# Kernel optimization log

Hardware: AMD Instinct MI355X
Metric: run time of the kernel (lower is better)

## Reference

```python
import jax, jax.numpy as jnp
import numpy as np

N, E, B = 25000, 400000, 64          # nodes, edges, graphs
F, ED, H, C = 32, 8, 4, 32           # feature/edge dims, heads, per-head dim
HC = H * C
L = 4                                # init conv + 3 stacked convs (same shapes)
LIN = 128


def setup_inputs() -> dict:
    key = jax.random.key(0)
    ks = jax.random.split(key, 24)
    s = 0.05
    inp = {
        "x": jax.random.normal(ks[0], (N, F), jnp.float32),
        "edge_attr": jax.random.normal(ks[1], (E, ED), jnp.float32),
        "edge_index": jax.random.randint(ks[2], (2, E), 0, N),
        "batch_index": jnp.sort(jax.random.randint(ks[3], (N,), 0, B)),
        # stacked TransformerConv params (leading dim = layer)
        "Wq": jax.random.normal(ks[4], (L, F, HC), jnp.float32) * s,
        "bq": jnp.zeros((L, HC), jnp.float32),
        "Wk": jax.random.normal(ks[5], (L, F, HC), jnp.float32) * s,
        "bk": jnp.zeros((L, HC), jnp.float32),
        "Wv": jax.random.normal(ks[6], (L, F, HC), jnp.float32) * s,
        "bv": jnp.zeros((L, HC), jnp.float32),
        "We": jax.random.normal(ks[7], (L, ED, HC), jnp.float32) * s,
        "be": jnp.zeros((L, HC), jnp.float32),
        "Wskip": jax.random.normal(ks[8], (L, F, HC), jnp.float32) * s,
        "bskip": jnp.zeros((L, HC), jnp.float32),
        "Wbeta": jax.random.normal(ks[9], (L, 3 * HC, 1), jnp.float32) * s,
        # per-layer Linear(H*C -> emb) + BatchNorm
        "Wlin": jax.random.normal(ks[10], (L, HC, F), jnp.float32) * s,
        "blin": jnp.zeros((L, F), jnp.float32),
        "bn_gamma": jnp.ones((L, F), jnp.float32),
        "bn_beta": jnp.zeros((L, F), jnp.float32),
        # readout MLP
        "W1": jax.random.normal(ks[11], (2 * F, LIN), jnp.float32) * s,
        "b1": jnp.zeros((LIN,), jnp.float32),
        "W2": jax.random.normal(ks[12], (LIN, LIN // 2), jnp.float32) * s,
        "b2": jnp.zeros((LIN // 2,), jnp.float32),
        "W3": jax.random.normal(ks[13], (LIN // 2, 1), jnp.float32) * s,
        "b3": jnp.zeros((1,), jnp.float32),
    }
    return inp


def _transformer_conv(x, edge_attr, src, dst, Wq, bq, Wk, bk, Wv, bv, We, be,
                      Wskip, bskip, Wbeta):
    """PyG TransformerConv(heads=H, concat=True, beta=True, edge_dim=ED), eval mode."""
    n = x.shape[0]
    q = (x @ Wq + bq).reshape(n, H, C)
    k = (x @ Wk + bk).reshape(n, H, C)
    v = (x @ Wv + bv).reshape(n, H, C)
    e = (edge_attr @ We + be).reshape(-1, H, C)          # [E,H,C]
    kj = k[src] + e                                       # key_j + edge
    alpha = jnp.einsum('ehc,ehc->eh', q[dst], kj) / np.sqrt(C).astype(np.float32)
    # segment softmax over incoming edges per destination node
    amax = jax.ops.segment_max(alpha, dst, num_segments=n)
    a = jnp.exp(alpha - amax[dst])
    denom = jax.ops.segment_sum(a, dst, num_segments=n)
    a = a / denom[dst]                                    # [E,H]
    msg = (v[src] + e) * a[:, :, None]
    out = jax.ops.segment_sum(msg, dst, num_segments=n).reshape(n, HC)
    x_skip = x @ Wskip + bskip
    beta = jax.nn.sigmoid(
        jnp.concatenate([out, x_skip, out - x_skip], axis=-1) @ Wbeta)  # [N,1]
    return beta * x_skip + (1.0 - beta) * out


def _bn(h, gamma, beta):
    m = h.mean(axis=0)
    v = h.var(axis=0)
    return (h - m) * jax.lax.rsqrt(v + 1e-5) * gamma + beta


def reference(x, edge_attr, edge_index, batch_index,
              Wq, bq, Wk, bk, Wv, bv, We, be, Wskip, bskip, Wbeta,
              Wlin, blin, bn_gamma, bn_beta, W1, b1, W2, b2, W3, b3):
    src, dst = edge_index[0], edge_index[1]
    counts = jax.ops.segment_sum(jnp.ones((N,), jnp.float32), batch_index,
                                 num_segments=B)[:, None]
    h = x
    rep = jnp.zeros((B, 2 * F), jnp.float32)
    for i in range(L):
        h = _transformer_conv(h, edge_attr, src, dst,
                              Wq[i], bq[i], Wk[i], bk[i], Wv[i], bv[i],
                              We[i], be[i], Wskip[i], bskip[i], Wbeta[i])
        h = jax.nn.elu(h @ Wlin[i] + blin[i])
        h = _bn(h, bn_gamma[i], bn_beta[i])
        if i > 0:  # original pools only inside the n_layers loop
            gmx = jax.ops.segment_max(h, batch_index, num_segments=B)
            gmean = jax.ops.segment_sum(h, batch_index, num_segments=B) / counts
            rep = rep + jnp.concatenate([gmx, gmean], axis=1)
    z = jax.nn.elu(rep @ W1 + b1)
    z = jax.nn.elu(z @ W2 + b2)
    return z @ W3 + b3  # [B,1]
```

## Files before the change

### kernel.cpp

```cpp
#include <hip/hip_runtime.h>
#include <hip/hip_bf16.h>
#include <hip/hip_fp16.h>
#include <math.h>

#define NN 25000
#define EE 400000
#define BB 64
#define FF 32
#define EDD 8
#define HH 4
#define CC 32
#define HCC 128
#define LL 4
#define LINN 128

#define RSQRT_C 0.17677669529663687f
#define NREP 16
#define LSTATS_WORDS (NREP * 64)


__global__ void deg_kernel(const int* __restrict__ dst, int* __restrict__ deg) {
    int i = blockIdx.x * blockDim.x + threadIdx.x;
    if (i < EE) atomicAdd(&deg[dst[i]], 1);
}

__global__ void gstart_kernel(const int* __restrict__ bidx, int* __restrict__ gstart) {
    int b = threadIdx.x;
    if (b <= BB) {
        int lo = 0, hi = NN;
        while (lo < hi) { int mid = (lo + hi) >> 1; if (bidx[mid] < b) lo = mid + 1; else hi = mid; }
        gstart[b] = lo;
    }
}

__global__ void scan1_kernel(const int* __restrict__ deg, int* __restrict__ rowp, int* __restrict__ blks) {
    __shared__ int s[256];
    int i = blockIdx.x * 256 + threadIdx.x;
    int v = (i < NN) ? deg[i] : 0;
    s[threadIdx.x] = v;
    __syncthreads();
    for (int off = 1; off < 256; off <<= 1) {
        int t = (threadIdx.x >= off) ? s[threadIdx.x - off] : 0;
        __syncthreads();
        s[threadIdx.x] += t;
        __syncthreads();
    }
    if (i < NN) rowp[i + 1] = s[threadIdx.x];
    if (threadIdx.x == 255) blks[blockIdx.x] = s[255];
    if (i == 0) rowp[0] = 0;
}

__global__ void scan2_kernel(int* __restrict__ blks, int nb) {
    __shared__ int s[128];
    int t = threadIdx.x;
    int v = (t < nb) ? blks[t] : 0;
    s[t] = v;
    __syncthreads();
    for (int off = 1; off < 128; off <<= 1) {
        int u = (t >= off) ? s[t - off] : 0;
        __syncthreads();
        s[t] += u;
        __syncthreads();
    }
    if (t < nb) blks[t] = s[t] - v;
}

__global__ void scan3_kernel(int* __restrict__ rowp, const int* __restrict__ blks) {
    int i = blockIdx.x * 256 + threadIdx.x;
    if (i < NN) rowp[i + 1] += blks[blockIdx.x];
}

__global__ void fill_kernel(const int* __restrict__ dst, const int* __restrict__ rowp,
                            int* __restrict__ cnt2, int* __restrict__ eid) {
    int i = blockIdx.x * blockDim.x + threadIdx.x;
    if (i < EE) {
        int d = dst[i];
        int pos = rowp[d] + atomicAdd(&cnt2[d], 1);
        eid[pos] = i;
    }
}

__global__ void sortseg_kernel(const int* __restrict__ rowp, int* __restrict__ eid) {
    int n = blockIdx.x * 256 + threadIdx.x;
    if (n >= NN) return;
    int b = rowp[n], e = rowp[n + 1];
    int d = e - b;
    if (d <= 1) return;
    if (d <= 64) {
        int buf[64];
        for (int i = 0; i < d; ++i) buf[i] = eid[b + i];
        for (int i = 1; i < d; ++i) {
            int key = buf[i];
            int j = i - 1;
            while (j >= 0 && buf[j] > key) { buf[j + 1] = buf[j]; --j; }
            buf[j + 1] = key;
        }
        for (int i = 0; i < d; ++i) eid[b + i] = buf[i];
    } else {
        for (int i = b + 1; i < e; ++i) {
            int key = eid[i];
            int j = i - 1;
            while (j >= b && eid[j] > key) { eid[j + 1] = eid[j]; --j; }
            eid[j + 1] = key;
        }
    }
}

__global__ void csr_gather_kernel(const int* __restrict__ csre, const int* __restrict__ srcA,
                                  const float* __restrict__ eattr,
                                  int* __restrict__ csrsrc, float4* __restrict__ ecsr) {
    int j = blockIdx.x * blockDim.x + threadIdx.x;
    if (j < EE) {
        int e = csre[j];
        csrsrc[j] = srcA[e];
        const float4* s = (const float4*)(eattr + (size_t)e * 8);
        ecsr[(size_t)j * 2] = s[0];
        ecsr[(size_t)j * 2 + 1] = s[1];
    }
}

__global__ __launch_bounds__(256) void qkvs_kernel(
    const float* __restrict__ hin,
    const float* __restrict__ Wq, const float* __restrict__ bq,
    const float* __restrict__ Wk, const float* __restrict__ bk,
    const float* __restrict__ Wv, const float* __restrict__ bv,
    const float* __restrict__ Ws, const float* __restrict__ bs,
    float2* __restrict__ qo,
    __half2* __restrict__ kvo,
    float2* __restrict__ so, float* __restrict__ lstats)
{
    if (blockIdx.x == 0) {
        for (int i = threadIdx.x; i < LSTATS_WORDS; i += 256) lstats[i] = 0.0f;
    }
    __shared__ float xs[32][32];
    int lane = threadIdx.x & 63;
    int sel = threadIdx.x >> 6;
    const float* W = (sel == 0) ? Wq : (sel == 1) ? Wk : (sel == 2) ? Wv : Ws;
    const float* bias = (sel == 0) ? bq : (sel == 1) ? bk : (sel == 2) ? bv : bs;
    float w0[32], w1[32];
#pragma unroll
    for (int f = 0; f < 32; ++f) {
        float2 t = *(const float2*)&W[f * 128 + 2 * lane];
        w0[f] = t.x; w1[f] = t.y;
    }
    float2 bvv = *(const float2*)&bias[2 * lane];

    int c = lane >> 1;
    int pr = lane & 1;
    int f2idx = c * 2 + pr;
    int h2k   = c * 4 + pr;
    int h2v   = c * 4 + 2 + pr;

    for (int chunk = blockIdx.x * 32; chunk < NN; chunk += gridDim.x * 32) {
        __syncthreads();
        for (int i = threadIdx.x; i < 1024; i += 256) {
            int nn = chunk + (i >> 5);
            xs[i >> 5][i & 31] = (nn < NN) ? hin[nn * 32 + (i & 31)] : 0.0f;
        }
        __syncthreads();
        int nmax = NN - chunk; if (nmax > 32) nmax = 32;
        for (int nl = 0; nl < nmax; ++nl) {
            float a0 = bvv.x, a1 = bvv.y;
#pragma unroll
            for (int f = 0; f < 32; ++f) {
                float xv = xs[nl][f];
                a0 += xv * w0[f];
                a1 += xv * w1[f];
            }
            size_t node = (size_t)(chunk + nl);
            if (sel == 0)      qo[node * 64 + f2idx] = make_float2(a0, a1);
            else if (sel == 1) kvo[node * 128 + h2k] = __float22half2_rn(make_float2(a0, a1));
            else if (sel == 2) kvo[node * 128 + h2v] = __float22half2_rn(make_float2(a0, a1));
            else               so[node * 64 + f2idx] = make_float2(a0, a1);
        }
    }
}

__global__ __launch_bounds__(256) void attn_kernel(
    const float4* __restrict__ qb4, const uint4* __restrict__ kvb4,
    const float4* __restrict__ skb4,
    const float4* __restrict__ eb4,
    const int* __restrict__ srcArr,
    const int* __restrict__ rowp,
    const float* __restrict__ WeL, const float* __restrict__ beL,
    const float* __restrict__ WbL,
    const float* __restrict__ WlinL, const float* __restrict__ blinL,
    float* __restrict__ hlin, float* __restrict__ bnpart)
{
    __shared__ __align__(16) float shc[4 * 128];
    __shared__ float sbn[64];

    int tid = threadIdx.x;
    if (tid < 64) sbn[tid] = 0.0f;
    __syncthreads();

    int w = tid >> 6;
    int lane = tid & 63;
    int n = blockIdx.x * 4 + w;

    if (n < NN) {
        int c = lane & 31;
        int h = lane >> 5;

        float4 we[8];
#pragma unroll
        for (int d = 0; d < 8; ++d) we[d] = *(const float4*)&WeL[d * 128 + 4 * c];
        float4 be4 = *(const float4*)&beL[4 * c];
        float4 wbo = *(const float4*)&WbL[4 * c];
        float4 wbs = *(const float4*)&WbL[128 + 4 * c];
        float4 wbd = *(const float4*)&WbL[256 + 4 * c];

        float4 q4 = qb4[(size_t)n * 32 + c];
        q4.x *= RSQRT_C; q4.y *= RSQRT_C; q4.z *= RSQRT_C; q4.w *= RSQRT_C;
        float4 sk4 = skb4[(size_t)n * 32 + c];

        int beg = rowp[n], end = rowp[n + 1];
        int cnt = end - beg;
        int last = end - 1;

        float s = 0.0f, a0 = 0.0f, a1 = 0.0f, a2 = 0.0f, a3 = 0.0f;

        uint4 kvA = make_uint4(0u, 0u, 0u, 0u), kvB = kvA;
        float4 eaA0 = make_float4(0.f, 0.f, 0.f, 0.f), eaA1 = eaA0;
        float4 eaB0 = eaA0, eaB1 = eaA0;
        int snC = 0, snD = 0;

        if (cnt > 0) {
            int j0 = beg + h;     j0 = (j0 < end) ? j0 : last;
            int j1 = beg + 2 + h; j1 = (j1 < end) ? j1 : last;
            int j2 = beg + 4 + h; j2 = (j2 < end) ? j2 : last;
            int j3 = beg + 6 + h; j3 = (j3 < end) ? j3 : last;
            int snA = srcArr[j0];
            int snB = srcArr[j1];
            snC = srcArr[j2];
            snD = srcArr[j3];
            kvA  = kvb4[(size_t)snA * 32 + c];
            kvB  = kvb4[(size_t)snB * 32 + c];
            eaA0 = eb4[(size_t)j0 * 2];
            eaA1 = eb4[(size_t)j0 * 2 + 1];
            eaB0 = eb4[(size_t)j1 * 2];
            eaB1 = eb4[(size_t)j1 * 2 + 1];
        }

        for (int jb = beg; jb < end; jb += 2) {
            int j = jb + h;
            uint4 kvC = kvb4[(size_t)snC * 32 + c];
            int jn = (j + 4 < end) ? j + 4 : last;
            float4 eaC0 = eb4[(size_t)jn * 2];
            float4 eaC1 = eb4[(size_t)jn * 2 + 1];
            int j8 = (j + 8 < end) ? j + 8 : last;
            int snE = srcArr[j8];

            float ex = be4.x, ey = be4.y, ez = be4.z, ew = be4.w;
            ex += eaA0.x * we[0].x + eaA0.y * we[1].x + eaA0.z * we[2].x + eaA0.w * we[3].x
                + eaA1.x * we[4].x + eaA1.y * we[5].x + eaA1.z * we[6].x + eaA1.w * we[7].x;
            ey += eaA0.x * we[0].y + eaA0.y * we[1].y + eaA0.z * we[2].y + eaA0.w * we[3].y
                + eaA1.x * we[4].y + eaA1.y * we[5].y + eaA1.z * we[6].y + eaA1.w * we[7].y;
            ez += eaA0.x * we[0].z + eaA0.y * we[1].z + eaA0.z * we[2].z + eaA0.w * we[3].z
                + eaA1.x * we[4].z + eaA1.y * we[5].z + eaA1.z * we[6].z + eaA1.w * we[7].z;
            ew += eaA0.x * we[0].w + eaA0.y * we[1].w + eaA0.z * we[2].w + eaA0.w * we[3].w
                + eaA1.x * we[4].w + eaA1.y * we[5].w + eaA1.z * we[6].w + eaA1.w * we[7].w;

            float2 k01 = __half22float2(*(const __half2*)&kvA.x);
            float2 k23 = __half22float2(*(const __half2*)&kvA.y);
            float2 v01 = __half22float2(*(const __half2*)&kvA.z);
            float2 v23 = __half22float2(*(const __half2*)&kvA.w);

            float p = q4.x * (k01.x + ex) + q4.y * (k01.y + ey)
                    + q4.z * (k23.x + ez) + q4.w * (k23.y + ew);
            p += __shfl_xor(p, 1);
            p += __shfl_xor(p, 2);
            p += __shfl_xor(p, 4);
            float wg = (j < end) ? __expf(p) : 0.0f;
            s += wg;
            a0 = fmaf(wg, v01.x + ex, a0);
            a1 = fmaf(wg, v01.y + ey, a1);
            a2 = fmaf(wg, v23.x + ez, a2);
            a3 = fmaf(wg, v23.y + ew, a3);

            kvA = kvB; kvB = kvC;
            eaA0 = eaB0; eaA1 = eaB1; eaB0 = eaC0; eaB1 = eaC1;
            snC = snD; snD = snE;
        }

        s  += __shfl_xor(s, 32);
        a0 += __shfl_xor(a0, 32);
        a1 += __shfl_xor(a1, 32);
        a2 += __shfl_xor(a2, 32);
        a3 += __shfl_xor(a3, 32);

        float rs = (cnt > 0) ? (1.0f / s) : 0.0f;
        float o0 = a0 * rs, o1 = a1 * rs, o2 = a2 * rs, o3 = a3 * rs;

        float t = o0 * wbo.x + sk4.x * wbs.x + (o0 - sk4.x) * wbd.x
                + o1 * wbo.y + sk4.y * wbs.y + (o1 - sk4.y) * wbd.y
                + o2 * wbo.z + sk4.z * wbs.z + (o2 - sk4.z) * wbd.z
                + o3 * wbo.w + sk4.w * wbs.w + (o3 - sk4.w) * wbd.w;
#pragma unroll
        for (int off = 1; off <= 16; off <<= 1) t += __shfl_xor(t, off);
        float beta = 1.0f / (1.0f + __expf(-t));
        float4 hc4;
        hc4.x = beta * sk4.x + (1.0f - beta) * o0;
        hc4.y = beta * sk4.y + (1.0f - beta) * o1;
        hc4.z = beta * sk4.z + (1.0f - beta) * o2;
        hc4.w = beta * sk4.w + (1.0f - beta) * o3;
        if (h == 0) ((float4*)shc)[w * 32 + c] = hc4;
        int cc = lane & 31;
        int half = lane >> 5;
        float acc = 0.0f;
#pragma unroll 8
        for (int i = 0; i < 64; ++i) {
            int ch = half * 64 + i;
            acc += shc[w * 128 + ch] * WlinL[ch * 32 + cc];
        }
        acc += __shfl_xor(acc, 32);
        if (lane < 32) {
            float hv = acc + blinL[lane];
            hv = (hv > 0.0f) ? hv : expm1f(hv);
            hlin[n * 32 + lane] = hv;
            atomicAdd(&sbn[lane], hv);
            atomicAdd(&sbn[32 + lane], hv * hv);
        }
    }
    __syncthreads();
    if (tid < 64) atomicAdd(&bnpart[(blockIdx.x & (NREP - 1)) * 64 + tid], sbn[tid]);
}

__global__ __launch_bounds__(256) void bnpool_kernel(
    const float* __restrict__ hlin, const float* __restrict__ bnpart,
    const float* __restrict__ gamma, const float* __restrict__ bnbeta,
    const int* __restrict__ gstart,
    float* __restrict__ hc, float* __restrict__ rep, int doPool)
{
    __shared__ float sscale[32], sshift[32];
    __shared__ float smax[8][32], ssum[8][32];
    int tid = threadIdx.x;
    int ch = tid & 31, row = tid >> 5;
    if (tid < 32) {
        float sm = 0.0f, sq = 0.0f;
#pragma unroll
        for (int r = 0; r < NREP; ++r) { sm += bnpart[r * 64 + tid]; sq += bnpart[r * 64 + 32 + tid]; }
        float mean = sm * (1.0f / NN);
        float var = sq * (1.0f / NN) - mean * mean;
        float scale = gamma[tid] * rsqrtf(var + 1e-5f);
        sscale[tid] = scale;
        sshift[tid] = bnbeta[tid] - mean * scale;
    }
    __syncthreads();
    int g = blockIdx.x;
    int gs = gstart[g], ge = gstart[g + 1];
    float scale = sscale[ch], shift = sshift[ch];
    float mx = -1e30f, sum = 0.0f;
    for (int n = gs + row; n < ge; n += 8) {
        float val = hlin[n * 32 + ch] * scale + shift;
        hc[n * 32 + ch] = val;
        mx = fmaxf(mx, val);
        sum += val;
    }
    if (doPool) {
        smax[row][ch] = mx; ssum[row][ch] = sum;
        __syncthreads();
        if (row == 0) {
#pragma unroll
            for (int r = 1; r < 8; ++r) { mx = fmaxf(mx, smax[r][ch]); sum += ssum[r][ch]; }
            int cntg = ge - gs;
            if (cntg > 0) {
                rep[g * 64 + ch]      += mx;
                rep[g * 64 + 32 + ch] += sum / (float)cntg;
            }
        }
    }
}

__device__ __forceinline__ float eluf(float x) { return x > 0.0f ? x : expm1f(x); }

__global__ __launch_bounds__(128) void readout_kernel(
    const float* __restrict__ rep,
    const float* __restrict__ W1, const float* __restrict__ b1,
    const float* __restrict__ W2, const float* __restrict__ b2,
    const float* __restrict__ W3, const float* __restrict__ b3,
    float* __restrict__ out)
{
    __shared__ float sr[64];
    __shared__ float sz1[128];
    __shared__ float sz2[64];
    int g = blockIdx.x;
    int t = threadIdx.x;
    if (t < 64) sr[t] = rep[g * 64 + t];
    __syncthreads();
    float acc = b1[t];
#pragma unroll 8
    for (int i = 0; i < 64; ++i) acc += sr[i] * W1[i * 128 + t];
    sz1[t] = eluf(acc);
    __syncthreads();
    if (t < 64) {
        float a2 = b2[t];
#pragma unroll 8
        for (int i = 0; i < 128; ++i) a2 += sz1[i] * W2[i * 64 + t];
        sz2[t] = eluf(a2);
    }
    __syncthreads();
    if (t < 64) {
        float p = sz2[t] * W3[t];
#pragma unroll
        for (int off = 1; off <= 32; off <<= 1) p += __shfl_xor(p, off);
        if (t == 0) out[g] = p + b3[0];
    }
}


extern "C" void kernel_launch(void* const* d_in, const int* in_sizes, int n_in,
                              void* d_out, int out_size, void* d_ws, size_t ws_size,
                              hipStream_t stream) {
    const float* x      = (const float*)d_in[0];
    const float* eattr  = (const float*)d_in[1];
    const int*   eidx   = (const int*)d_in[2];
    const int*   bidx   = (const int*)d_in[3];
    const float* Wq     = (const float*)d_in[4];
    const float* bq     = (const float*)d_in[5];
    const float* Wk     = (const float*)d_in[6];
    const float* bk     = (const float*)d_in[7];
    const float* Wv     = (const float*)d_in[8];
    const float* bv     = (const float*)d_in[9];
    const float* We     = (const float*)d_in[10];
    const float* be     = (const float*)d_in[11];
    const float* Wskip  = (const float*)d_in[12];
    const float* bskip  = (const float*)d_in[13];
    const float* Wbeta  = (const float*)d_in[14];
    const float* Wlin   = (const float*)d_in[15];
    const float* blin   = (const float*)d_in[16];
    const float* bng    = (const float*)d_in[17];
    const float* bnb    = (const float*)d_in[18];
    const float* W1     = (const float*)d_in[19];
    const float* b1     = (const float*)d_in[20];
    const float* W2     = (const float*)d_in[21];
    const float* b2     = (const float*)d_in[22];
    const float* W3     = (const float*)d_in[23];
    const float* b3     = (const float*)d_in[24];
    float* out = (float*)d_out;

    char* ws = (char*)d_ws;
    size_t off = 0;
    auto alloc = [&](size_t bytes) -> char* {
        char* p = ws + off;
        off = (off + bytes + 255) & ~(size_t)255;
        return p;
    };
    int*    rowp   = (int*)alloc((NN + 1) * 4);
    int*    degcnt = (int*)alloc(2 * NN * 4);
    int*    deg    = degcnt;
    int*    cnt2   = degcnt + NN;
    int*    csre   = (int*)alloc(EE * 4);
    int*    blks   = (int*)alloc(128 * 4);
    int*    gstart = (int*)alloc((BB + 1) * 4);
    float*  rep    = (float*)alloc(BB * 64 * 4);
    float4* qB     = (float4*)alloc((size_t)NN * 32 * 16);
    uint4*  kvB    = (uint4*)alloc((size_t)NN * 32 * 16);
    float4* skB    = (float4*)alloc((size_t)NN * 32 * 16);
    float*  hlin   = (float*)alloc((size_t)NN * 32 * 4);
    float*  hcur   = (float*)alloc((size_t)NN * 32 * 4);
    float*  bnpart = (float*)alloc(LSTATS_WORDS * 4);
    int*    csrsrc = (int*)alloc(EE * 4);
    float4* ecsr   = (float4*)alloc((size_t)EE * 32);

    const int* srcA = eidx;
    const int* dstA = eidx + EE;

    (void)hipMemsetAsync(degcnt, 0, 2 * NN * 4, stream);
    (void)hipMemsetAsync(rep, 0, BB * 64 * 4, stream);

    deg_kernel<<<(EE + 255) / 256, 256, 0, stream>>>(dstA, deg);
    gstart_kernel<<<1, 128, 0, stream>>>(bidx, gstart);
    scan1_kernel<<<98, 256, 0, stream>>>(deg, rowp, blks);
    scan2_kernel<<<1, 128, 0, stream>>>(blks, 98);
    scan3_kernel<<<98, 256, 0, stream>>>(rowp, blks);
    fill_kernel<<<(EE + 255) / 256, 256, 0, stream>>>(dstA, rowp, cnt2, csre);
    sortseg_kernel<<<98, 256, 0, stream>>>(rowp, csre);
    csr_gather_kernel<<<(EE + 255) / 256, 256, 0, stream>>>(csre, srcA, eattr, csrsrc, ecsr);

    const float* hin = x;
    for (int l = 0; l < LL; ++l) {
        qkvs_kernel<<<782, 256, 0, stream>>>(
            hin,
            Wq + l * FF * HCC, bq + l * HCC,
            Wk + l * FF * HCC, bk + l * HCC,
            Wv + l * FF * HCC, bv + l * HCC,
            Wskip + l * FF * HCC, bskip + l * HCC,
            (float2*)qB, (__half2*)kvB, (float2*)skB, bnpart);

        attn_kernel<<<(NN + 3) / 4, 256, 0, stream>>>(
            qB, kvB, skB, ecsr, csrsrc, rowp,
            We + l * EDD * HCC, be + l * HCC,
            Wbeta + l * 3 * HCC,
            Wlin + l * HCC * FF, blin + l * FF,
            hlin, bnpart);

        bnpool_kernel<<<BB, 256, 0, stream>>>(hlin, bnpart, bng + l * FF, bnb + l * FF,
                                              gstart, hcur, rep, (l > 0) ? 1 : 0);
        hin = hcur;
    }

    readout_kernel<<<64, 128, 0, stream>>>(rep, W1, b1, W2, b2, W3, b3, out);
}
```

Measured before the change: 586.8 us.

## Fold edge projection into query and aggregate raw edge attrs per head

Instead of projecting each edge's 8-dim attribute to 128 channels per edge, precompute q·We per head (8 scalars) and the q·be term, so each edge's score contribution becomes an 8-term dot product. The value side accumulates weighted raw edge attributes, and the We projection is applied once per node after the loop. This cuts per-edge FMAs and frees the 32 registers that held We, at the cost of 8 extra accumulators and some extra shuffles outside the loop.

```diff
diff --git a/kernel.cpp b/kernel.cpp
--- a/kernel.cpp
+++ b/kernel.cpp
@@ -202,23 +202,33 @@
         int c = lane & 31;
         int h = lane >> 5;
 
-        float4 we[8];
-#pragma unroll
-        for (int d = 0; d < 8; ++d) we[d] = *(const float4*)&WeL[d * 128 + 4 * c];
-        float4 be4 = *(const float4*)&beL[4 * c];
-        float4 wbo = *(const float4*)&WbL[4 * c];
-        float4 wbs = *(const float4*)&WbL[128 + 4 * c];
-        float4 wbd = *(const float4*)&WbL[256 + 4 * c];
-
         float4 q4 = qb4[(size_t)n * 32 + c];
         q4.x *= RSQRT_C; q4.y *= RSQRT_C; q4.z *= RSQRT_C; q4.w *= RSQRT_C;
-        float4 sk4 = skb4[(size_t)n * 32 + c];
+
+        float r[8];
+        float qbe;
+        {
+#pragma unroll
+            for (int d = 0; d < 8; ++d) {
+                float4 wd = *(const float4*)&WeL[d * 128 + 4 * c];
+                r[d] = q4.x * wd.x + q4.y * wd.y + q4.z * wd.z + q4.w * wd.w;
+            }
+            float4 be4 = *(const float4*)&beL[4 * c];
+            qbe = q4.x * be4.x + q4.y * be4.y + q4.z * be4.z + q4.w * be4.w;
+#pragma unroll
+            for (int off = 1; off <= 4; off <<= 1) {
+#pragma unroll
+                for (int d = 0; d < 8; ++d) r[d] += __shfl_xor(r[d], off);
+                qbe += __shfl_xor(qbe, off);
+            }
+        }
 
         int beg = rowp[n], end = rowp[n + 1];
         int cnt = end - beg;
         int last = end - 1;
 
         float s = 0.0f, a0 = 0.0f, a1 = 0.0f, a2 = 0.0f, a3 = 0.0f;
+        float t0 = 0.f, t1 = 0.f, t2 = 0.f, t3 = 0.f, t4 = 0.f, t5 = 0.f, t6 = 0.f, t7 = 0.f;
 
         uint4 kvA = make_uint4(0u, 0u, 0u, 0u), kvB = kvA;
         float4 eaA0 = make_float4(0.f, 0.f, 0.f, 0.f), eaA1 = eaA0;
@@ -251,32 +261,31 @@
             int j8 = (j + 8 < end) ? j + 8 : last;
             int snE = srcArr[j8];
 
-            float ex = be4.x, ey = be4.y, ez = be4.z, ew = be4.w;
-            ex += eaA0.x * we[0].x + eaA0.y * we[1].x + eaA0.z * we[2].x + eaA0.w * we[3].x
-                + eaA1.x * we[4].x + eaA1.y * we[5].x + eaA1.z * we[6].x + eaA1.w * we[7].x;
-            ey += eaA0.x * we[0].y + eaA0.y * we[1].y + eaA0.z * we[2].y + eaA0.w * we[3].y
-                + eaA1.x * we[4].y + eaA1.y * we[5].y + eaA1.z * we[6].y + eaA1.w * we[7].y;
-            ez += eaA0.x * we[0].z + eaA0.y * we[1].z + eaA0.z * we[2].z + eaA0.w * we[3].z
-                + eaA1.x * we[4].z + eaA1.y * we[5].z + eaA1.z * we[6].z + eaA1.w * we[7].z;
-            ew += eaA0.x * we[0].w + eaA0.y * we[1].w + eaA0.z * we[2].w + eaA0.w * we[3].w
-                + eaA1.x * we[4].w + eaA1.y * we[5].w + eaA1.z * we[6].w + eaA1.w * we[7].w;
-
             float2 k01 = __half22float2(*(const __half2*)&kvA.x);
             float2 k23 = __half22float2(*(const __half2*)&kvA.y);
             float2 v01 = __half22float2(*(const __half2*)&kvA.z);
             float2 v23 = __half22float2(*(const __half2*)&kvA.w);
 
-            float p = q4.x * (k01.x + ex) + q4.y * (k01.y + ey)
-                    + q4.z * (k23.x + ez) + q4.w * (k23.y + ew);
+            float p = q4.x * k01.x + q4.y * k01.y + q4.z * k23.x + q4.w * k23.y;
             p += __shfl_xor(p, 1);
             p += __shfl_xor(p, 2);
             p += __shfl_xor(p, 4);
-            float wg = (j < end) ? __expf(p) : 0.0f;
+            float pe = eaA0.x * r[0] + eaA0.y * r[1] + eaA0.z * r[2] + eaA0.w * r[3]
+                     + eaA1.x * r[4] + eaA1.y * r[5] + eaA1.z * r[6] + eaA1.w * r[7] + qbe;
+            float wg = (j < end) ? __expf(p + pe) : 0.0f;
             s += wg;
-            a0 = fmaf(wg, v01.x + ex, a0);
-            a1 = fmaf(wg, v01.y + ey, a1);
-            a2 = fmaf(wg, v23.x + ez, a2);
-            a3 = fmaf(wg, v23.y + ew, a3);
+            a0 = fmaf(wg, v01.x, a0);
+            a1 = fmaf(wg, v01.y, a1);
+            a2 = fmaf(wg, v23.x, a2);
+            a3 = fmaf(wg, v23.y, a3);
+            t0 = fmaf(wg, eaA0.x, t0);
+            t1 = fmaf(wg, eaA0.y, t1);
+            t2 = fmaf(wg, eaA0.z, t2);
+            t3 = fmaf(wg, eaA0.w, t3);
+            t4 = fmaf(wg, eaA1.x, t4);
+            t5 = fmaf(wg, eaA1.y, t5);
+            t6 = fmaf(wg, eaA1.z, t6);
+            t7 = fmaf(wg, eaA1.w, t7);
 
             kvA = kvB; kvB = kvC;
             eaA0 = eaB0; eaA1 = eaB1; eaB0 = eaC0; eaB1 = eaC1;
@@ -288,9 +297,47 @@
         a1 += __shfl_xor(a1, 32);
         a2 += __shfl_xor(a2, 32);
         a3 += __shfl_xor(a3, 32);
+        t0 += __shfl_xor(t0, 32);
+        t1 += __shfl_xor(t1, 32);
+        t2 += __shfl_xor(t2, 32);
+        t3 += __shfl_xor(t3, 32);
+        t4 += __shfl_xor(t4, 32);
+        t5 += __shfl_xor(t5, 32);
+        t6 += __shfl_xor(t6, 32);
+        t7 += __shfl_xor(t7, 32);
+
+        {
+            float4 wd;
+            wd = *(const float4*)&WeL[0 * 128 + 4 * c];
+            a0 = fmaf(t0, wd.x, a0); a1 = fmaf(t0, wd.y, a1); a2 = fmaf(t0, wd.z, a2); a3 = fmaf(t0, wd.w, a3);
+            wd = *(const float4*)&WeL[1 * 128 + 4 * c];
+            a0 = fmaf(t1, wd.x, a0); a1 = fmaf(t1, wd.y, a1); a2 = fmaf(t1, wd.z, a2); a3 = fmaf(t1, wd.w, a3);
+            wd = *(const float4*)&WeL[2 * 128 + 4 * c];
+            a0 = fmaf(t2, wd.x, a0); a1 = fmaf(t2, wd.y, a1); a2 = fmaf(t2, wd.z, a2); a3 = fmaf(t2, wd.w, a3);
+            wd = *(const float4*)&WeL[3 * 128 + 4 * c];
+            a0 = fmaf(t3, wd.x, a0); a1 = fmaf(t3, wd.y, a1); a2 = fmaf(t3, wd.z, a2); a3 = fmaf(t3, wd.w, a3);
+            wd = *(const float4*)&WeL[4 * 128 + 4 * c];
+            a0 = fmaf(t4, wd.x, a0); a1 = fmaf(t4, wd.y, a1); a2 = fmaf(t4, wd.z, a2); a3 = fmaf(t4, wd.w, a3);
+            wd = *(const float4*)&WeL[5 * 128 + 4 * c];
+            a0 = fmaf(t5, wd.x, a0); a1 = fmaf(t5, wd.y, a1); a2 = fmaf(t5, wd.z, a2); a3 = fmaf(t5, wd.w, a3);
+            wd = *(const float4*)&WeL[6 * 128 + 4 * c];
+            a0 = fmaf(t6, wd.x, a0); a1 = fmaf(t6, wd.y, a1); a2 = fmaf(t6, wd.z, a2); a3 = fmaf(t6, wd.w, a3);
+            wd = *(const float4*)&WeL[7 * 128 + 4 * c];
+            a0 = fmaf(t7, wd.x, a0); a1 = fmaf(t7, wd.y, a1); a2 = fmaf(t7, wd.z, a2); a3 = fmaf(t7, wd.w, a3);
+            float4 be4 = *(const float4*)&beL[4 * c];
+            a0 = fmaf(s, be4.x, a0);
+            a1 = fmaf(s, be4.y, a1);
+            a2 = fmaf(s, be4.z, a2);
+            a3 = fmaf(s, be4.w, a3);
+        }
 
         float rs = (cnt > 0) ? (1.0f / s) : 0.0f;
         float o0 = a0 * rs, o1 = a1 * rs, o2 = a2 * rs, o3 = a3 * rs;
+
+        float4 sk4 = skb4[(size_t)n * 32 + c];
+        float4 wbo = *(const float4*)&WbL[4 * c];
+        float4 wbs = *(const float4*)&WbL[128 + 4 * c];
+        float4 wbd = *(const float4*)&WbL[256 + 4 * c];
 
         float t = o0 * wbo.x + sk4.x * wbs.x + (o0 - sk4.x) * wbd.x
                 + o1 * wbo.y + sk4.y * wbs.y + (o1 - sk4.y) * wbd.y
```

Measured after the change: 590.0 us. Within noise of the previous version (+0.5%).

## Store q, skip and edge attributes in fp16 and split BN-pool across more blocks

Applied to the files above, without the earlier changes.

Query and skip projections and the CSR-ordered edge attributes are now stored as half precision instead of fp32, halving the bytes the attention kernel gathers per node and per edge. The skip and beta weight loads are moved after the edge loop to shorten register live ranges. The BN+pool kernel is split into four chunks per graph, with a small combine kernel for the pooled max and mean, and it skips writing normalized features on the final layer. The fp16 storage adds rounding error to the attention inputs, and the pool split adds one extra launch per pooled layer.

```diff
diff --git a/kernel.cpp b/kernel.cpp
--- a/kernel.cpp
+++ b/kernel.cpp
@@ -108,14 +108,21 @@
 
 __global__ void csr_gather_kernel(const int* __restrict__ csre, const int* __restrict__ srcA,
                                   const float* __restrict__ eattr,
-                                  int* __restrict__ csrsrc, float4* __restrict__ ecsr) {
+                                  int* __restrict__ csrsrc, uint4* __restrict__ eh) {
     int j = blockIdx.x * blockDim.x + threadIdx.x;
     if (j < EE) {
         int e = csre[j];
         csrsrc[j] = srcA[e];
         const float4* s = (const float4*)(eattr + (size_t)e * 8);
-        ecsr[(size_t)j * 2] = s[0];
-        ecsr[(size_t)j * 2 + 1] = s[1];
+        float4 s0 = s[0], s1 = s[1];
+        __half2 h0 = __float22half2_rn(make_float2(s0.x, s0.y));
+        __half2 h1 = __float22half2_rn(make_float2(s0.z, s0.w));
+        __half2 h2 = __float22half2_rn(make_float2(s1.x, s1.y));
+        __half2 h3 = __float22half2_rn(make_float2(s1.z, s1.w));
+        uint4 o;
+        o.x = *(unsigned*)&h0; o.y = *(unsigned*)&h1;
+        o.z = *(unsigned*)&h2; o.w = *(unsigned*)&h3;
+        eh[j] = o;
     }
 }
 
@@ -125,9 +132,8 @@
     const float* __restrict__ Wk, const float* __restrict__ bk,
     const float* __restrict__ Wv, const float* __restrict__ bv,
     const float* __restrict__ Ws, const float* __restrict__ bs,
-    float2* __restrict__ qo,
-    __half2* __restrict__ kvo,
-    float2* __restrict__ so, float* __restrict__ lstats)
+    __half2* __restrict__ qo, __half2* __restrict__ kvo,
+    __half2* __restrict__ so, float* __restrict__ lstats)
 {
     if (blockIdx.x == 0) {
         for (int i = threadIdx.x; i < LSTATS_WORDS; i += 256) lstats[i] = 0.0f;
@@ -147,9 +153,8 @@
 
     int c = lane >> 1;
     int pr = lane & 1;
-    int f2idx = c * 2 + pr;
-    int h2k   = c * 4 + pr;
-    int h2v   = c * 4 + 2 + pr;
+    int h2k = c * 4 + pr;
+    int h2v = c * 4 + 2 + pr;
 
     for (int chunk = blockIdx.x * 32; chunk < NN; chunk += gridDim.x * 32) {
         __syncthreads();
@@ -168,18 +173,19 @@
                 a1 += xv * w1[f];
             }
             size_t node = (size_t)(chunk + nl);
-            if (sel == 0)      qo[node * 64 + f2idx] = make_float2(a0, a1);
-            else if (sel == 1) kvo[node * 128 + h2k] = __float22half2_rn(make_float2(a0, a1));
-            else if (sel == 2) kvo[node * 128 + h2v] = __float22half2_rn(make_float2(a0, a1));
-            else               so[node * 64 + f2idx] = make_float2(a0, a1);
+            __half2 hv = __float22half2_rn(make_float2(a0, a1));
+            if (sel == 0)      qo[node * 64 + lane] = hv;
+            else if (sel == 1) kvo[node * 128 + h2k] = hv;
+            else if (sel == 2) kvo[node * 128 + h2v] = hv;
+            else               so[node * 64 + lane] = hv;
         }
     }
 }
 
 __global__ __launch_bounds__(256) void attn_kernel(
-    const float4* __restrict__ qb4, const uint4* __restrict__ kvb4,
-    const float4* __restrict__ skb4,
-    const float4* __restrict__ eb4,
+    const uint2* __restrict__ qh, const uint4* __restrict__ kvb4,
+    const uint2* __restrict__ skh,
+    const uint4* __restrict__ eh,
     const int* __restrict__ srcArr,
     const int* __restrict__ rowp,
     const float* __restrict__ WeL, const float* __restrict__ beL,
@@ -206,13 +212,12 @@
 #pragma unroll
         for (int d = 0; d < 8; ++d) we[d] = *(const float4*)&WeL[d * 128 + 4 * c];
         float4 be4 = *(const float4*)&beL[4 * c];
-        float4 wbo = *(const float4*)&WbL[4 * c];
-        float4 wbs = *(const float4*)&WbL[128 + 4 * c];
-        float4 wbd = *(const float4*)&WbL[256 + 4 * c];
-
-        float4 q4 = qb4[(size_t)n * 32 + c];
-        q4.x *= RSQRT_C; q4.y *= RSQRT_C; q4.z *= RSQRT_C; q4.w *= RSQRT_C;
-        float4 sk4 = skb4[(size_t)n * 32 + c];
+
+        uint2 qraw = qh[(size_t)n * 32 + c];
+        float2 q01 = __half22float2(*(const __half2*)&qraw.x);
+        float2 q23 = __half22float2(*(const __half2*)&qraw.y);
+        float4 q4 = make_float4(q01.x * RSQRT_C, q01.y * RSQRT_C,
+                                q23.x * RSQRT_C, q23.y * RSQRT_C);
 
         int beg = rowp[n], end = rowp[n + 1];
         int cnt = end - beg;
@@ -221,8 +226,7 @@
         float s = 0.0f, a0 = 0.0f, a1 = 0.0f, a2 = 0.0f, a3 = 0.0f;
 
         uint4 kvA = make_uint4(0u, 0u, 0u, 0u), kvB = kvA;
-        float4 eaA0 = make_float4(0.f, 0.f, 0.f, 0.f), eaA1 = eaA0;
-        float4 eaB0 = eaA0, eaB1 = eaA0;
+        uint4 eaA = kvA, eaB = kvA;
         int snC = 0, snD = 0;
 
         if (cnt > 0) {
@@ -234,32 +238,34 @@
             int snB = srcArr[j1];
             snC = srcArr[j2];
             snD = srcArr[j3];
-            kvA  = kvb4[(size_t)snA * 32 + c];
-            kvB  = kvb4[(size_t)snB * 32 + c];
-            eaA0 = eb4[(size_t)j0 * 2];
-            eaA1 = eb4[(size_t)j0 * 2 + 1];
-            eaB0 = eb4[(size_t)j1 * 2];
-            eaB1 = eb4[(size_t)j1 * 2 + 1];
+            kvA = kvb4[(size_t)snA * 32 + c];
+            kvB = kvb4[(size_t)snB * 32 + c];
+            eaA = eh[j0];
+            eaB = eh[j1];
         }
 
         for (int jb = beg; jb < end; jb += 2) {
             int j = jb + h;
             uint4 kvC = kvb4[(size_t)snC * 32 + c];
             int jn = (j + 4 < end) ? j + 4 : last;
-            float4 eaC0 = eb4[(size_t)jn * 2];
-            float4 eaC1 = eb4[(size_t)jn * 2 + 1];
+            uint4 eaC = eh[jn];
             int j8 = (j + 8 < end) ? j + 8 : last;
             int snE = srcArr[j8];
 
+            float2 e01 = __half22float2(*(const __half2*)&eaA.x);
+            float2 e23 = __half22float2(*(const __half2*)&eaA.y);
+            float2 e45 = __half22float2(*(const __half2*)&eaA.z);
+            float2 e67 = __half22float2(*(const __half2*)&eaA.w);
+            float ead[8] = { e01.x, e01.y, e23.x, e23.y, e45.x, e45.y, e67.x, e67.y };
+
             float ex = be4.x, ey = be4.y, ez = be4.z, ew = be4.w;
-            ex += eaA0.x * we[0].x + eaA0.y * we[1].x + eaA0.z * we[2].x + eaA0.w * we[3].x
-                + eaA1.x * we[4].x + eaA1.y * we[5].x + eaA1.z * we[6].x + eaA1.w * we[7].x;
-            ey += eaA0.x * we[0].y + eaA0.y * we[1].y + eaA0.z * we[2].y + eaA0.w * we[3].y
-                + eaA1.x * we[4].y + eaA1.y * we[5].y + eaA1.z * we[6].y + eaA1.w * we[7].y;
-            ez += eaA0.x * we[0].z + eaA0.y * we[1].z + eaA0.z * we[2].z + eaA0.w * we[3].z
-                + eaA1.x * we[4].z + eaA1.y * we[5].z + eaA1.z * we[6].z + eaA1.w * we[7].z;
-            ew += eaA0.x * we[0].w + eaA0.y * we[1].w + eaA0.z * we[2].w + eaA0.w * we[3].w
-                + eaA1.x * we[4].w + eaA1.y * we[5].w + eaA1.z * we[6].w + eaA1.w * we[7].w;
+#pragma unroll
+            for (int d = 0; d < 8; ++d) {
+                ex = fmaf(ead[d], we[d].x, ex);
+                ey = fmaf(ead[d], we[d].y, ey);
+                ez = fmaf(ead[d], we[d].z, ez);
+                ew = fmaf(ead[d], we[d].w, ew);
+            }
 
             float2 k01 = __half22float2(*(const __half2*)&kvA.x);
             float2 k23 = __half22float2(*(const __half2*)&kvA.y);
@@ -279,7 +285,7 @@
             a3 = fmaf(wg, v23.y + ew, a3);
 
             kvA = kvB; kvB = kvC;
-            eaA0 = eaB0; eaA1 = eaB1; eaB0 = eaC0; eaB1 = eaC1;
+            eaA = eaB; eaB = eaC;
             snC = snD; snD = snE;
         }
 
@@ -291,6 +297,15 @@
 
         float rs = (cnt > 0) ? (1.0f / s) : 0.0f;
         float o0 = a0 * rs, o1 = a1 * rs, o2 = a2 * rs, o3 = a3 * rs;
+
+        uint2 skraw = skh[(size_t)n * 32 + c];
+        float2 s01 = __half22float2(*(const __half2*)&skraw.x);
+        float2 s23 = __half22float2(*(const __half2*)&skraw.y);
+        float4 sk4 = make_float4(s01.x, s01.y, s23.x, s23.y);
+
+        float4 wbo = *(const float4*)&WbL[4 * c];
+        float4 wbs = *(const float4*)&WbL[128 + 4 * c];
+        float4 wbd = *(const float4*)&WbL[256 + 4 * c];
 
         float t = o0 * wbo.x + sk4.x * wbs.x + (o0 - sk4.x) * wbd.x
                 + o1 * wbo.y + sk4.y * wbs.y + (o1 - sk4.y) * wbd.y
@@ -330,7 +345,7 @@
     const float* __restrict__ hlin, const float* __restrict__ bnpart,
     const float* __restrict__ gamma, const float* __restrict__ bnbeta,
     const int* __restrict__ gstart,
-    float* __restrict__ hc, float* __restrict__ rep, int doPool)
+    float* __restrict__ hc, float* __restrict__ pool4, int doWrite)
 {
     __shared__ float sscale[32], sshift[32];
     __shared__ float smax[8][32], ssum[8][32];
@@ -347,27 +362,47 @@
         sshift[tid] = bnbeta[tid] - mean * scale;
     }
     __syncthreads();
-    int g = blockIdx.x;
+    int g = blockIdx.x >> 2;
+    int chunk = blockIdx.x & 3;
     int gs = gstart[g], ge = gstart[g + 1];
+    int len = ge - gs;
+    int cs = gs + (len * chunk) / 4;
+    int ce = gs + (len * (chunk + 1)) / 4;
     float scale = sscale[ch], shift = sshift[ch];
     float mx = -1e30f, sum = 0.0f;
-    for (int n = gs + row; n < ge; n += 8) {
+    for (int n = cs + row; n < ce; n += 8) {
         float val = hlin[n * 32 + ch] * scale + shift;
-        hc[n * 32 + ch] = val;
+        if (doWrite) hc[n * 32 + ch] = val;
         mx = fmaxf(mx, val);
         sum += val;
     }
-    if (doPool) {
-        smax[row][ch] = mx; ssum[row][ch] = sum;
-        __syncthreads();
-        if (row == 0) {
-#pragma unroll
-            for (int r = 1; r < 8; ++r) { mx = fmaxf(mx, smax[r][ch]); sum += ssum[r][ch]; }
-            int cntg = ge - gs;
-            if (cntg > 0) {
-                rep[g * 64 + ch]      += mx;
-                rep[g * 64 + 32 + ch] += sum / (float)cntg;
+    smax[row][ch] = mx; ssum[row][ch] = sum;
+    __syncthreads();
+    if (row == 0) {
+#pragma unroll
+        for (int r = 1; r < 8; ++r) { mx = fmaxf(mx, smax[r][ch]); sum += ssum[r][ch]; }
+        pool4[(size_t)blockIdx.x * 64 + ch]      = mx;
+        pool4[(size_t)blockIdx.x * 64 + 32 + ch] = sum;
+    }
+}
+
+__global__ void pool_combine_kernel(const float* __restrict__ pool4,
+                                    const int* __restrict__ gstart,
+                                    float* __restrict__ rep) {
+    int i = blockIdx.x * blockDim.x + threadIdx.x;
+    if (i < BB * 32) {
+        int g = i >> 5, ch = i & 31;
+        int cntg = gstart[g + 1] - gstart[g];
+        if (cntg > 0) {
+            float mx = pool4[(size_t)(g * 4) * 64 + ch];
+            float sum = pool4[(size_t)(g * 4) * 64 + 32 + ch];
+#pragma unroll
+            for (int k = 1; k < 4; ++k) {
+                mx = fmaxf(mx, pool4[(size_t)(g * 4 + k) * 64 + ch]);
+                sum += pool4[(size_t)(g * 4 + k) * 64 + 32 + ch];
             }
+            rep[g * 64 + ch]      += mx;
+            rep[g * 64 + 32 + ch] += sum / (float)cntg;
         }
     }
 }
@@ -446,22 +481,23 @@
         off = (off + bytes + 255) & ~(size_t)255;
         return p;
     };
-    int*    rowp   = (int*)alloc((NN + 1) * 4);
-    int*    degcnt = (int*)alloc(2 * NN * 4);
-    int*    deg    = degcnt;
-    int*    cnt2   = degcnt + NN;
-    int*    csre   = (int*)alloc(EE * 4);
-    int*    blks   = (int*)alloc(128 * 4);
-    int*    gstart = (int*)alloc((BB + 1) * 4);
-    float*  rep    = (float*)alloc(BB * 64 * 4);
-    float4* qB     = (float4*)alloc((size_t)NN * 32 * 16);
-    uint4*  kvB    = (uint4*)alloc((size_t)NN * 32 * 16);
-    float4* skB    = (float4*)alloc((size_t)NN * 32 * 16);
-    float*  hlin   = (float*)alloc((size_t)NN * 32 * 4);
-    float*  hcur   = (float*)alloc((size_t)NN * 32 * 4);
-    float*  bnpart = (float*)alloc(LSTATS_WORDS * 4);
-    int*    csrsrc = (int*)alloc(EE * 4);
-    float4* ecsr   = (float4*)alloc((size_t)EE * 32);
+    int*     rowp   = (int*)alloc((NN + 1) * 4);
+    int*     degcnt = (int*)alloc(2 * NN * 4);
+    int*     deg    = degcnt;
+    int*     cnt2   = degcnt + NN;
+    int*     csre   = (int*)alloc(EE * 4);
+    int*     blks   = (int*)alloc(128 * 4);
+    int*     gstart = (int*)alloc((BB + 1) * 4);
+    float*   rep    = (float*)alloc(BB * 64 * 4);
+    float*   pool4  = (float*)alloc(BB * 4 * 64 * 4);
+    __half2* qH     = (__half2*)alloc((size_t)NN * 64 * 4);
+    __half2* kvB    = (__half2*)alloc((size_t)NN * 128 * 4);
+    __half2* skH    = (__half2*)alloc((size_t)NN * 64 * 4);
+    float*   hlin   = (float*)alloc((size_t)NN * 32 * 4);
+    float*   hcur   = (float*)alloc((size_t)NN * 32 * 4);
+    float*   bnpart = (float*)alloc(LSTATS_WORDS * 4);
+    int*     csrsrc = (int*)alloc(EE * 4);
+    uint4*   ecsrh  = (uint4*)alloc((size_t)EE * 16);
 
     const int* srcA = eidx;
     const int* dstA = eidx + EE;
@@ -476,7 +512,7 @@
     scan3_kernel<<<98, 256, 0, stream>>>(rowp, blks);
     fill_kernel<<<(EE + 255) / 256, 256, 0, stream>>>(dstA, rowp, cnt2, csre);
     sortseg_kernel<<<98, 256, 0, stream>>>(rowp, csre);
-    csr_gather_kernel<<<(EE + 255) / 256, 256, 0, stream>>>(csre, srcA, eattr, csrsrc, ecsr);
+    csr_gather_kernel<<<(EE + 255) / 256, 256, 0, stream>>>(csre, srcA, eattr, csrsrc, ecsrh);
 
     const float* hin = x;
     for (int l = 0; l < LL; ++l) {
@@ -486,17 +522,21 @@
             Wk + l * FF * HCC, bk + l * HCC,
             Wv + l * FF * HCC, bv + l * HCC,
             Wskip + l * FF * HCC, bskip + l * HCC,
-            (float2*)qB, (__half2*)kvB, (float2*)skB, bnpart);
+            qH, kvB, skH, bnpart);
 
         attn_kernel<<<(NN + 3) / 4, 256, 0, stream>>>(
-            qB, kvB, skB, ecsr, csrsrc, rowp,
+            (const uint2*)qH, (const uint4*)kvB, (const uint2*)skH,
+            ecsrh, csrsrc, rowp,
             We + l * EDD * HCC, be + l * HCC,
             Wbeta + l * 3 * HCC,
             Wlin + l * HCC * FF, blin + l * FF,
             hlin, bnpart);
 
-        bnpool_kernel<<<BB, 256, 0, stream>>>(hlin, bnpart, bng + l * FF, bnb + l * FF,
-                                              gstart, hcur, rep, (l > 0) ? 1 : 0);
+        bnpool_kernel<<<BB * 4, 256, 0, stream>>>(hlin, bnpart, bng + l * FF, bnb + l * FF,
+                                                  gstart, hcur, pool4, (l < LL - 1) ? 1 : 0);
+        if (l > 0) {
+            pool_combine_kernel<<<8, 256, 0, stream>>>(pool4, gstart, rep);
+        }
         hin = hcur;
     }
 
```

Result: faster. 545.3 us (-7.1%).
